# Kernel tuning notes

Measured on AMD Instinct MI355X. Metric: run time of the kernel, lower is better.

Reference implementation:

```python
import jax, jax.numpy as jnp
import numpy as np

N = 100000
E = 1600000
IN_DIM = 128
HID = 64
HEADS = 1
NEG_SLOPE = 0.2


def setup_inputs() -> dict:
    key = jax.random.key(0)
    ks = jax.random.split(key, 12)
    x = jax.random.normal(ks[0], (N, IN_DIM), dtype=jnp.float32)
    edge_index = jax.random.randint(ks[1], (2, E), 0, N, dtype=jnp.int64)
    s1 = 1.0 / np.sqrt(IN_DIM)
    s2 = 1.0 / np.sqrt(HEADS * HID)
    return {
        "x": x,
        "edge_index": edge_index,
        # layer 1: in_dim -> heads*hid
        "W1": jax.random.normal(ks[2], (IN_DIM, HEADS * HID), dtype=jnp.float32) * s1,
        "a_src1": jax.random.normal(ks[3], (HEADS, HID), dtype=jnp.float32) * s1,
        "a_dst1": jax.random.normal(ks[4], (HEADS, HID), dtype=jnp.float32) * s1,
        "b1": jnp.zeros((HEADS * HID,), dtype=jnp.float32),
        # layer 2: heads*hid -> hid (1 head)
        "W2": jax.random.normal(ks[5], (HEADS * HID, HID), dtype=jnp.float32) * s2,
        "a_src2": jax.random.normal(ks[6], (1, HID), dtype=jnp.float32) * s2,
        "a_dst2": jax.random.normal(ks[7], (1, HID), dtype=jnp.float32) * s2,
        "b2": jnp.zeros((HID,), dtype=jnp.float32),
        # output head
        "W_out": jax.random.normal(ks[8], (HID, 1), dtype=jnp.float32) * (1.0 / np.sqrt(HID)),
        "b_out": jnp.zeros((1,), dtype=jnp.float32),
    }


def _gat_conv(x, src, dst, W, a_src, a_dst, bias, heads, hid):
    n = x.shape[0]
    h = (x @ W).reshape(n, heads, hid)                      # [N, H, D]
    alpha_s = jnp.einsum("nhd,hd->nh", h, a_src)            # [N, H]
    alpha_d = jnp.einsum("nhd,hd->nh", h, a_dst)
    e = alpha_s[src] + alpha_d[dst]                          # [E, H]
    e = jax.nn.leaky_relu(e, NEG_SLOPE)
    # segment softmax over edges sharing the same destination node
    m = jax.ops.segment_max(e, dst, num_segments=n)          # [N, H]
    ex = jnp.exp(e - m[dst])
    denom = jax.ops.segment_sum(ex, dst, num_segments=n)     # [N, H]
    alpha = ex / denom[dst]                                  # [E, H]
    out = jax.ops.segment_sum(h[src] * alpha[:, :, None], dst, num_segments=n)
    return out.reshape(n, heads * hid) + bias


def reference(x, edge_index, W1, a_src1, a_dst1, b1, W2, a_src2, a_dst2, b2, W_out, b_out):
    n = x.shape[0]
    # PyG GATConv default add_self_loops=True
    loops = jnp.arange(n, dtype=edge_index.dtype)
    src = jnp.concatenate([edge_index[0], loops])
    dst = jnp.concatenate([edge_index[1], loops])
    h = jax.nn.elu(_gat_conv(x, src, dst, W1, a_src1, a_dst1, b1, HEADS, HID))
    h = jax.nn.elu(_gat_conv(h, src, dst, W2, a_src2, a_dst2, b2, 1, HID))
    return (h @ W_out + b_out).squeeze(-1)                   # [N]
```

## Files before the change

kernel.cpp:

```cpp
#include <hip/hip_runtime.h>
#include <hip/hip_fp16.h>
#include <math.h>

#define NEG_SLOPE 0.2f
#define BKT_SHIFT 8
#define BKT_NODES (1 << BKT_SHIFT)
#define BKT_CAP 512
#define BKT_FCAP 6144
#define BKT_SHARD (BKT_FCAP / 4)
#define P1_CHUNK 4096

typedef _Float16 f16x8 __attribute__((ext_vector_type(8)));
typedef float    f32x4 __attribute__((ext_vector_type(4)));
union FU  { uint4 u; f16x8 f; };
union H2U { __half2 h; unsigned u; };

__device__ __forceinline__ float lrelu(float x){ return fmaxf(x, NEG_SLOPE * x); }
__device__ __forceinline__ float elu_fast(float x){
  float t = __expf(fminf(x, 0.f)) - 1.f;
  return x > 0.f ? x : t;
}


__global__ __launch_bounds__(256) void k_p1(const int* __restrict__ src, const int* __restrict__ dst,
                                            int E, int B, int* __restrict__ bktCur,
                                            unsigned* __restrict__ pairs,
                                            const float* __restrict__ W1, const float* __restrict__ W2,
                                            uint4* __restrict__ W1f, uint4* __restrict__ W2f){
  __shared__ int h[BKT_CAP], base[BKT_CAP], cur[BKT_CAP];
  int tid = threadIdx.x;
  if (blockIdx.x == 0){
    for (int idx = tid; idx < 16 * 64; idx += 256){
      int lane = idx & 63, fs = idx >> 6;
      int t = fs >> 2, s = fs & 3;
      int m = lane & 15, quad = lane >> 4;
      f16x8 v;
      #pragma unroll
      for (int j = 0; j < 8; ++j)
        v[j] = (_Float16)W1[(s * 32 + quad * 8 + j) * 64 + t * 16 + m];
      FU fu; fu.f = v;
      W1f[fs * 64 + lane] = fu.u;
    }
    for (int idx = tid; idx < 8 * 64; idx += 256){
      int lane = idx & 63, fs = idx >> 6;
      int t = fs >> 1, s = fs & 1;
      int m = lane & 15, quad = lane >> 4;
      f16x8 v;
      #pragma unroll
      for (int j = 0; j < 8; ++j)
        v[j] = (_Float16)W2[(s * 32 + quad * 8 + j) * 64 + t * 16 + m];
      FU fu; fu.f = v;
      W2f[fs * 64 + lane] = fu.u;
    }
  }
  for (int i = tid; i < BKT_CAP; i += 256){ h[i] = 0; cur[i] = 0; }
  __syncthreads();
  int beg = blockIdx.x * P1_CHUNK;
  int end = min(beg + P1_CHUNK, E);
  int shard = blockIdx.x & 3;
  int m4 = (end - beg) >> 2;
  const int4* d4 = (const int4*)(dst + beg);
  const int4* s4 = (const int4*)(src + beg);
  for (int i = tid; i < m4; i += 256){
    int4 d = d4[i];
    atomicAdd(&h[d.x >> BKT_SHIFT], 1); atomicAdd(&h[d.y >> BKT_SHIFT], 1);
    atomicAdd(&h[d.z >> BKT_SHIFT], 1); atomicAdd(&h[d.w >> BKT_SHIFT], 1);
  }
  for (int i = beg + (m4 << 2) + tid; i < end; i += 256)
    atomicAdd(&h[dst[i] >> BKT_SHIFT], 1);
  __syncthreads();
  for (int i = tid; i < B; i += 256)
    if (h[i]) base[i] = i * BKT_FCAP + shard * BKT_SHARD + atomicAdd(&bktCur[i * 4 + shard], h[i]);
  __syncthreads();
  for (int i = tid; i < m4; i += 256){
    int4 d = d4[i]; int4 s = s4[i];
    int b0 = d.x >> BKT_SHIFT, b1 = d.y >> BKT_SHIFT, b2 = d.z >> BKT_SHIFT, b3 = d.w >> BKT_SHIFT;
    int p0 = base[b0] + atomicAdd(&cur[b0], 1);
    pairs[p0] = ((unsigned)(d.x & (BKT_NODES-1)) << 17) | (unsigned)s.x;
    int p1 = base[b1] + atomicAdd(&cur[b1], 1);
    pairs[p1] = ((unsigned)(d.y & (BKT_NODES-1)) << 17) | (unsigned)s.y;
    int p2 = base[b2] + atomicAdd(&cur[b2], 1);
    pairs[p2] = ((unsigned)(d.z & (BKT_NODES-1)) << 17) | (unsigned)s.z;
    int p3 = base[b3] + atomicAdd(&cur[b3], 1);
    pairs[p3] = ((unsigned)(d.w & (BKT_NODES-1)) << 17) | (unsigned)s.w;
  }
  for (int i = beg + (m4 << 2) + tid; i < end; i += 256){
    int d = dst[i], s = src[i];
    int b = d >> BKT_SHIFT;
    int p = base[b] + atomicAdd(&cur[b], 1);
    pairs[p] = ((unsigned)(d & (BKT_NODES-1)) << 17) | (unsigned)s;
  }
}

__device__ __forceinline__ void p2_body(const unsigned* __restrict__ pairs,
                                        const int* __restrict__ bktCur,
                                        int N, int2* __restrict__ offs2, int* __restrict__ col, int b){
  __shared__ int sc[BKT_NODES], cu[BKT_NODES];
  int tid = threadIdx.x;
  int nbase = b << BKT_SHIFT;
  int bs = b * BKT_FCAP;
  sc[tid] = 0;
  __syncthreads();
  #pragma unroll
  for (int s = 0; s < 4; ++s){
    int ss_ = bs + s * BKT_SHARD;
    int se_ = ss_ + bktCur[b * 4 + s];
    for (int i = ss_ + tid; i < se_; i += 256)
      atomicAdd(&sc[pairs[i] >> 17], 1);
  }
  __syncthreads();
  int v = sc[tid];
  for (int o = 1; o < 256; o <<= 1){
    int x = (tid >= o) ? sc[tid - o] : 0;
    __syncthreads();
    sc[tid] += x;
    __syncthreads();
  }
  int ex = sc[tid] - v;
  cu[tid] = bs + ex;
  if (nbase + tid < N) offs2[nbase + tid] = make_int2(bs + ex, bs + ex + v);
  __syncthreads();
  #pragma unroll
  for (int s = 0; s < 4; ++s){
    int ss_ = bs + s * BKT_SHARD;
    int se_ = ss_ + bktCur[b * 4 + s];
    for (int i = ss_ + tid; i < se_; i += 256){
      unsigned pr = pairs[i];
      int p = atomicAdd(&cu[pr >> 17], 1);
      col[p] = (int)(pr & 0x1FFFFu);
    }
  }
}

__device__ __forceinline__ void mg1_body(
    const float* __restrict__ X, const uint4* __restrict__ Wf,
    const float* __restrict__ a_src, const float* __restrict__ a_dst,
    uint2* __restrict__ H, float* __restrict__ as_, float* __restrict__ ad_, int n, int bb)
{
  int lane = threadIdx.x & 63, wv = threadIdx.x >> 6;
  int quad = lane >> 4, nn = lane & 15;
  int rowb = bb * 64 + wv * 16;
  int row = rowb + nn;
  bool ok = row < n;
  int rowc = ok ? row : n - 1;

  f16x8 af[4][4];
  #pragma unroll
  for (int t = 0; t < 4; ++t)
    #pragma unroll
    for (int s = 0; s < 4; ++s){
      FU fu; fu.u = Wf[(t * 4 + s) * 64 + lane];
      af[t][s] = fu.f;
    }

  const float4* Xr = (const float4*)(X + (size_t)rowc * 128);
  float4 xb[4][2];
  #pragma unroll
  for (int s = 0; s < 4; ++s){
    xb[s][0] = Xr[s * 8 + quad * 2];
    xb[s][1] = Xr[s * 8 + quad * 2 + 1];
  }

  f32x4 acc[4] = {};
  #pragma unroll
  for (int s = 0; s < 4; ++s){
    f16x8 bf;
    bf[0] = (_Float16)xb[s][0].x; bf[1] = (_Float16)xb[s][0].y;
    bf[2] = (_Float16)xb[s][0].z; bf[3] = (_Float16)xb[s][0].w;
    bf[4] = (_Float16)xb[s][1].x; bf[5] = (_Float16)xb[s][1].y;
    bf[6] = (_Float16)xb[s][1].z; bf[7] = (_Float16)xb[s][1].w;
    #pragma unroll
    for (int t = 0; t < 4; ++t)
      acc[t] = __builtin_amdgcn_mfma_f32_16x16x32_f16(af[t][s], bf, acc[t], 0, 0, 0);
  }

  if (ok){
    #pragma unroll
    for (int t = 0; t < 4; ++t){
      H2U p0, p1;
      p0.h = __floats2half2_rn(acc[t][0], acc[t][1]);
      p1.h = __floats2half2_rn(acc[t][2], acc[t][3]);
      H[(size_t)row * 16 + t * 4 + quad] = make_uint2(p0.u, p1.u);
    }
  }
  float sl = 0.f, dl = 0.f;
  #pragma unroll
  for (int t = 0; t < 4; ++t){
    float4 a4 = ((const float4*)a_src)[t * 4 + quad];
    float4 d4 = ((const float4*)a_dst)[t * 4 + quad];
    sl += acc[t][0] * a4.x + acc[t][1] * a4.y + acc[t][2] * a4.z + acc[t][3] * a4.w;
    dl += acc[t][0] * d4.x + acc[t][1] * d4.y + acc[t][2] * d4.z + acc[t][3] * d4.w;
  }
  sl += __shfl_xor(sl, 16, 64); sl += __shfl_xor(sl, 32, 64);
  dl += __shfl_xor(dl, 16, 64); dl += __shfl_xor(dl, 32, 64);
  if (lane < 16 && ok){ as_[row] = sl; ad_[row] = dl; }
}

__global__ __launch_bounds__(256) void k_fused(
    const unsigned* __restrict__ pairs, const int* __restrict__ bktCur,
    int N, int2* __restrict__ offs2, int* __restrict__ col, int p2B,
    const float* __restrict__ X, const uint4* __restrict__ Wf,
    const float* __restrict__ a_src, const float* __restrict__ a_dst,
    uint2* __restrict__ H, float* __restrict__ as_, float* __restrict__ ad_)
{
  if ((int)blockIdx.x < p2B)
    p2_body(pairs, bktCur, N, offs2, col, blockIdx.x);
  else
    mg1_body(X, Wf, a_src, a_dst, H, as_, ad_, N, blockIdx.x - p2B);
}

#define FMA8(e, hv) { const __half2* hp = (const __half2*)&(hv);               \
  a[0]=fmaf(e, __half2float(hp[0].x), a[0]); a[1]=fmaf(e, __half2float(hp[0].y), a[1]); \
  a[2]=fmaf(e, __half2float(hp[1].x), a[2]); a[3]=fmaf(e, __half2float(hp[1].y), a[3]); \
  a[4]=fmaf(e, __half2float(hp[2].x), a[4]); a[5]=fmaf(e, __half2float(hp[2].y), a[5]); \
  a[6]=fmaf(e, __half2float(hp[3].x), a[6]); a[7]=fmaf(e, __half2float(hp[3].y), a[7]); }

__device__ __forceinline__ void agg_core(
    const int2* __restrict__ offs2, const int* __restrict__ col,
    const uint4* __restrict__ H4, const float* __restrict__ as_, const float* __restrict__ ad_,
    int node, int c8, float& denom, float a[8])
{
  int2 be2 = offs2[node];
  int beg = be2.x, d = be2.y - be2.x;
  int maxd = d;
  maxd = max(maxd, __shfl_xor(maxd, 8, 64));
  maxd = max(maxd, __shfl_xor(maxd, 16, 64));
  maxd = max(maxd, __shfl_xor(maxd, 32, 64));
  float adv = ad_[node];
  float exs = __expf(lrelu(as_[node] + adv));
  uint4 hself = H4[(size_t)node * 8 + c8];
  denom = exs;
  { const __half2* hp = (const __half2*)&hself;
    #pragma unroll
    for (int i = 0; i < 4; ++i){
      a[2*i]   = exs * __half2float(hp[i].x);
      a[2*i+1] = exs * __half2float(hp[i].y);
    } }
  for (int j = 0; j < maxd; j += 4){
    int ss[4]; float asv[4]; uint4 hv[4];
    #pragma unroll
    for (int u = 0; u < 4; ++u) ss[u] = (j + u < d) ? col[beg + j + u] : 0;
    #pragma unroll
    for (int u = 0; u < 4; ++u) asv[u] = as_[ss[u]];
    #pragma unroll
    for (int u = 0; u < 4; ++u) hv[u] = H4[(size_t)ss[u] * 8 + c8];
    #pragma unroll
    for (int u = 0; u < 4; ++u){
      float e = (j + u < d) ? __expf(lrelu(asv[u] + adv)) : 0.f;
      denom += e;
      FMA8(e, hv[u])
    }
  }
}

__global__ __launch_bounds__(256) void k_agg1f(
    const int2* __restrict__ offs2, const int* __restrict__ col,
    const uint4* __restrict__ H4, const float* __restrict__ as_, const float* __restrict__ ad_,
    const float* __restrict__ bias, const uint4* __restrict__ W2f,
    const float* __restrict__ a_src2, const float* __restrict__ a_dst2,
    uint2* __restrict__ H2out, float* __restrict__ as2_, float* __restrict__ ad2_, int n)
{
  __shared__ unsigned uhl[32][36];
  int lane = threadIdx.x & 63, w = threadIdx.x >> 6;
  int m = lane >> 3, c8 = lane & 7;
  int node0 = blockIdx.x * 32 + w * 8 + m;
  bool ok = node0 < n;
  int node = ok ? node0 : n - 1;
  float denom; float a[8];
  agg_core(offs2, col, H4, as_, ad_, node, c8, denom, a);
  float inv = 1.f / denom;
  float4 b0 = *(const float4*)&bias[8 * c8];
  float4 b1 = *(const float4*)&bias[8 * c8 + 4];
  float bb[8] = {b0.x, b0.y, b0.z, b0.w, b1.x, b1.y, b1.z, b1.w};
  int ln = w * 8 + m;
  #pragma unroll
  for (int i = 0; i < 4; ++i){
    float v0 = elu_fast(fmaf(a[2*i],   inv, bb[2*i]));
    float v1 = elu_fast(fmaf(a[2*i+1], inv, bb[2*i+1]));
    __half2 h = __floats2half2_rn(v0, v1);
    uhl[ln][c8 * 4 + i] = *(unsigned*)&h;
  }
  __syncthreads();

  if (w < 2){
    int quad = lane >> 4, nn = lane & 15;
    int lrow = w * 16 + nn;
    int row = blockIdx.x * 32 + lrow;
    bool ok2 = row < n;

    f16x8 af[4][2];
    #pragma unroll
    for (int t = 0; t < 4; ++t)
      #pragma unroll
      for (int s = 0; s < 2; ++s){
        FU fu; fu.u = W2f[(t * 2 + s) * 64 + lane];
        af[t][s] = fu.f;
      }

    f16x8 bf[2];
    #pragma unroll
    for (int s = 0; s < 2; ++s){
      FU fu; fu.u = ((const uint4*)&uhl[lrow][0])[s * 4 + quad];
      bf[s] = fu.f;
    }

    f32x4 acc[4] = {};
    #pragma unroll
    for (int s = 0; s < 2; ++s)
      #pragma unroll
      for (int t = 0; t < 4; ++t)
        acc[t] = __builtin_amdgcn_mfma_f32_16x16x32_f16(af[t][s], bf[s], acc[t], 0, 0, 0);

    if (ok2){
      #pragma unroll
      for (int t = 0; t < 4; ++t){
        H2U p0, p1;
        p0.h = __floats2half2_rn(acc[t][0], acc[t][1]);
        p1.h = __floats2half2_rn(acc[t][2], acc[t][3]);
        H2out[(size_t)row * 16 + t * 4 + quad] = make_uint2(p0.u, p1.u);
      }
    }
    float sl = 0.f, dl = 0.f;
    #pragma unroll
    for (int t = 0; t < 4; ++t){
      float4 a4 = ((const float4*)a_src2)[t * 4 + quad];
      float4 d4 = ((const float4*)a_dst2)[t * 4 + quad];
      sl += acc[t][0] * a4.x + acc[t][1] * a4.y + acc[t][2] * a4.z + acc[t][3] * a4.w;
      dl += acc[t][0] * d4.x + acc[t][1] * d4.y + acc[t][2] * d4.z + acc[t][3] * d4.w;
    }
    sl += __shfl_xor(sl, 16, 64); sl += __shfl_xor(sl, 32, 64);
    dl += __shfl_xor(dl, 16, 64); dl += __shfl_xor(dl, 32, 64);
    if (lane < 16 && ok2){ as2_[row] = sl; ad2_[row] = dl; }
  }
}

__global__ __launch_bounds__(256) void k_agg2(
    const int2* __restrict__ offs2, const int* __restrict__ col,
    const uint4* __restrict__ H4, const float* __restrict__ as_, const float* __restrict__ ad_,
    const float* __restrict__ bias, const float* __restrict__ Wout, const float* __restrict__ bout,
    float* __restrict__ out, int n)
{
  int lane = threadIdx.x & 63, w = threadIdx.x >> 6;
  int m = lane >> 3, c8 = lane & 7;
  int node0 = blockIdx.x * 32 + w * 8 + m;
  bool ok = node0 < n;
  int node = ok ? node0 : n - 1;
  float denom; float a[8];
  agg_core(offs2, col, H4, as_, ad_, node, c8, denom, a);
  float inv = 1.f / denom;
  float4 b0 = *(const float4*)&bias[8 * c8];
  float4 b1 = *(const float4*)&bias[8 * c8 + 4];
  float4 w0 = *(const float4*)&Wout[8 * c8];
  float4 w1 = *(const float4*)&Wout[8 * c8 + 4];
  float bb[8] = {b0.x, b0.y, b0.z, b0.w, b1.x, b1.y, b1.z, b1.w};
  float ww[8] = {w0.x, w0.y, w0.z, w0.w, w1.x, w1.y, w1.z, w1.w};
  float p = 0.f;
  #pragma unroll
  for (int i = 0; i < 8; ++i)
    p += elu_fast(fmaf(a[i], inv, bb[i])) * ww[i];
  p += __shfl_xor(p, 1, 64); p += __shfl_xor(p, 2, 64); p += __shfl_xor(p, 4, 64);
  if (c8 == 0 && ok) out[node] = p + bout[0];
}

extern "C" void kernel_launch(void* const* d_in, const int* in_sizes, int n_in,
                              void* d_out, int out_size, void* d_ws, size_t ws_size,
                              hipStream_t stream)
{
  const float* x    = (const float*)d_in[0];
  const int*   ei   = (const int*)d_in[1];
  const float* W1   = (const float*)d_in[2];
  const float* as1w = (const float*)d_in[3];
  const float* ad1w = (const float*)d_in[4];
  const float* b1   = (const float*)d_in[5];
  const float* W2   = (const float*)d_in[6];
  const float* as2w = (const float*)d_in[7];
  const float* ad2w = (const float*)d_in[8];
  const float* b2   = (const float*)d_in[9];
  const float* Wout = (const float*)d_in[10];
  const float* bout = (const float*)d_in[11];
  float* out = (float*)d_out;

  const int N = in_sizes[0] / 128;
  const int E = in_sizes[1] / 2;
  const int* srcA = ei;
  const int* dstA = ei + E;
  const int B = (N + BKT_NODES - 1) >> BKT_SHIFT;

  char* p = (char*)d_ws;
  auto alloc = [&](size_t bytes){ char* r = p; p += (bytes + 255) & ~255ull; return r; };
  int*   bktCur = (int*)alloc(BKT_CAP * 4 * 4);
  int2*  offs2  = (int2*)alloc((size_t)N * 8);
  int*   col    = (int*)alloc((size_t)B * BKT_FCAP * 4);
  float* vas1 = (float*)alloc((size_t)N * 4);
  float* vad1 = (float*)alloc((size_t)N * 4);
  float* vas2 = (float*)alloc((size_t)N * 4);
  float* vad2 = (float*)alloc((size_t)N * 4);
  uint4* w1f  = (uint4*)alloc(16 * 64 * 16);
  uint4* w2f  = (uint4*)alloc(8 * 64 * 16);
  uint2* h1   = (uint2*)alloc((size_t)N * 64 * 2);
  uint2* h2   = (uint2*)alloc((size_t)N * 64 * 2);
  unsigned* pairs = (unsigned*)h2;

  hipMemsetAsync(bktCur, 0, BKT_CAP * 4 * 4, stream);

  int nchunk = (E + P1_CHUNK - 1) / P1_CHUNK;
  k_p1<<<nchunk, 256, 0, stream>>>(srcA, dstA, E, B, bktCur, pairs, W1, W2, w1f, w2f);

  int gblocks = (N + 63) / 64;
  int ablocks = (N + 31) / 32;
  k_fused<<<B + gblocks, 256, 0, stream>>>(pairs, bktCur, N, offs2, col, B,
                                           x, w1f, as1w, ad1w, h1, vas1, vad1);
  k_agg1f <<<ablocks, 256, 0, stream>>>(offs2, col, (const uint4*)h1, vas1, vad1, b1,
                                        w2f, as2w, ad2w, h2, vas2, vad2, N);
  k_agg2  <<<ablocks, 256, 0, stream>>>(offs2, col, (const uint4*)h2, vas2, vad2, b2, Wout, bout, out, N);
}
```

Before: 234.8 us.

## Replace global bucket atomics with per-chunk local sort and offset table

The edge bucketing pass now sorts each chunk's edges by bucket in shared memory, using a block-wide prefix scan over a 512-entry histogram. It writes them contiguously per chunk together with a per-chunk bucket offset table, which removes the global atomic counters and the memset. The CSR build pass then gathers each bucket's segments from all chunks through that offset table into shared memory before counting and scattering. This replaces the scattered global writes with coalesced ones, at the cost of a per-bucket gather of roughly 391 short segments read serially by each thread, plus larger shared-memory staging.

```diff
diff --git a/kernel.cpp b/kernel.cpp
--- a/kernel.cpp
+++ b/kernel.cpp
@@ -5,9 +5,7 @@
 #define NEG_SLOPE 0.2f
 #define BKT_SHIFT 8
 #define BKT_NODES (1 << BKT_SHIFT)
-#define BKT_CAP 512
 #define BKT_FCAP 6144
-#define BKT_SHARD (BKT_FCAP / 4)
 #define P1_CHUNK 4096
 
 typedef _Float16 f16x8 __attribute__((ext_vector_type(8)));
@@ -21,16 +19,16 @@
   return x > 0.f ? x : t;
 }
 
-
-__global__ __launch_bounds__(256) void k_p1(const int* __restrict__ src, const int* __restrict__ dst,
-                                            int E, int B, int* __restrict__ bktCur,
-                                            unsigned* __restrict__ pairs,
+__global__ __launch_bounds__(512) void k_p1(const int* __restrict__ src, const int* __restrict__ dst,
+                                            int E, int B,
+                                            unsigned* __restrict__ pairs, int* __restrict__ offsT,
                                             const float* __restrict__ W1, const float* __restrict__ W2,
                                             uint4* __restrict__ W1f, uint4* __restrict__ W2f){
-  __shared__ int h[BKT_CAP], base[BKT_CAP], cur[BKT_CAP];
+  __shared__ int h[512], cur[512];
+  __shared__ unsigned stage[P1_CHUNK];
   int tid = threadIdx.x;
   if (blockIdx.x == 0){
-    for (int idx = tid; idx < 16 * 64; idx += 256){
+    for (int idx = tid; idx < 16 * 64; idx += 512){
       int lane = idx & 63, fs = idx >> 6;
       int t = fs >> 2, s = fs & 3;
       int m = lane & 15, quad = lane >> 4;
@@ -41,7 +39,7 @@
       FU fu; fu.f = v;
       W1f[fs * 64 + lane] = fu.u;
     }
-    for (int idx = tid; idx < 8 * 64; idx += 256){
+    for (int idx = tid; idx < 8 * 64; idx += 512){
       int lane = idx & 63, fs = idx >> 6;
       int t = fs >> 1, s = fs & 1;
       int m = lane & 15, quad = lane >> 4;
@@ -53,61 +51,84 @@
       W2f[fs * 64 + lane] = fu.u;
     }
   }
-  for (int i = tid; i < BKT_CAP; i += 256){ h[i] = 0; cur[i] = 0; }
+  h[tid] = 0;
   __syncthreads();
   int beg = blockIdx.x * P1_CHUNK;
   int end = min(beg + P1_CHUNK, E);
-  int shard = blockIdx.x & 3;
-  int m4 = (end - beg) >> 2;
+  int cnt = end - beg;
+  int m4 = cnt >> 2;
   const int4* d4 = (const int4*)(dst + beg);
   const int4* s4 = (const int4*)(src + beg);
-  for (int i = tid; i < m4; i += 256){
+  for (int i = tid; i < m4; i += 512){
     int4 d = d4[i];
     atomicAdd(&h[d.x >> BKT_SHIFT], 1); atomicAdd(&h[d.y >> BKT_SHIFT], 1);
     atomicAdd(&h[d.z >> BKT_SHIFT], 1); atomicAdd(&h[d.w >> BKT_SHIFT], 1);
   }
-  for (int i = beg + (m4 << 2) + tid; i < end; i += 256)
-    atomicAdd(&h[dst[i] >> BKT_SHIFT], 1);
-  __syncthreads();
-  for (int i = tid; i < B; i += 256)
-    if (h[i]) base[i] = i * BKT_FCAP + shard * BKT_SHARD + atomicAdd(&bktCur[i * 4 + shard], h[i]);
-  __syncthreads();
-  for (int i = tid; i < m4; i += 256){
+  for (int i = (m4 << 2) + tid; i < cnt; i += 512)
+    atomicAdd(&h[dst[beg + i] >> BKT_SHIFT], 1);
+  __syncthreads();
+  int v = h[tid];
+  for (int o = 1; o < 512; o <<= 1){
+    int x = (tid >= o) ? h[tid - o] : 0;
+    __syncthreads();
+    h[tid] += x;
+    __syncthreads();
+  }
+  int e = h[tid] - v;
+  cur[tid] = e;
+  int* orow = offsT + (size_t)blockIdx.x * (B + 1);
+  if (tid <= B) orow[tid] = e;
+  __syncthreads();
+  for (int i = tid; i < m4; i += 512){
     int4 d = d4[i]; int4 s = s4[i];
-    int b0 = d.x >> BKT_SHIFT, b1 = d.y >> BKT_SHIFT, b2 = d.z >> BKT_SHIFT, b3 = d.w >> BKT_SHIFT;
-    int p0 = base[b0] + atomicAdd(&cur[b0], 1);
-    pairs[p0] = ((unsigned)(d.x & (BKT_NODES-1)) << 17) | (unsigned)s.x;
-    int p1 = base[b1] + atomicAdd(&cur[b1], 1);
-    pairs[p1] = ((unsigned)(d.y & (BKT_NODES-1)) << 17) | (unsigned)s.y;
-    int p2 = base[b2] + atomicAdd(&cur[b2], 1);
-    pairs[p2] = ((unsigned)(d.z & (BKT_NODES-1)) << 17) | (unsigned)s.z;
-    int p3 = base[b3] + atomicAdd(&cur[b3], 1);
-    pairs[p3] = ((unsigned)(d.w & (BKT_NODES-1)) << 17) | (unsigned)s.w;
-  }
-  for (int i = beg + (m4 << 2) + tid; i < end; i += 256){
-    int d = dst[i], s = src[i];
-    int b = d >> BKT_SHIFT;
-    int p = base[b] + atomicAdd(&cur[b], 1);
-    pairs[p] = ((unsigned)(d & (BKT_NODES-1)) << 17) | (unsigned)s;
-  }
+    int p0 = atomicAdd(&cur[d.x >> BKT_SHIFT], 1);
+    stage[p0] = ((unsigned)(d.x & (BKT_NODES-1)) << 17) | (unsigned)s.x;
+    int p1 = atomicAdd(&cur[d.y >> BKT_SHIFT], 1);
+    stage[p1] = ((unsigned)(d.y & (BKT_NODES-1)) << 17) | (unsigned)s.y;
+    int p2 = atomicAdd(&cur[d.z >> BKT_SHIFT], 1);
+    stage[p2] = ((unsigned)(d.z & (BKT_NODES-1)) << 17) | (unsigned)s.z;
+    int p3 = atomicAdd(&cur[d.w >> BKT_SHIFT], 1);
+    stage[p3] = ((unsigned)(d.w & (BKT_NODES-1)) << 17) | (unsigned)s.w;
+  }
+  for (int i = (m4 << 2) + tid; i < cnt; i += 512){
+    int d = dst[beg + i], s = src[beg + i];
+    int p = atomicAdd(&cur[d >> BKT_SHIFT], 1);
+    stage[p] = ((unsigned)(d & (BKT_NODES-1)) << 17) | (unsigned)s;
+  }
+  __syncthreads();
+  unsigned* prow = pairs + (size_t)blockIdx.x * P1_CHUNK;
+  for (int i = tid; i < cnt; i += 512) prow[i] = stage[i];
 }
 
 __device__ __forceinline__ void p2_body(const unsigned* __restrict__ pairs,
-                                        const int* __restrict__ bktCur,
-                                        int N, int2* __restrict__ offs2, int* __restrict__ col, int b){
-  __shared__ int sc[BKT_NODES], cu[BKT_NODES];
+                                        const int* __restrict__ offsT,
+                                        int NCH, int B, int N,
+                                        int2* __restrict__ offs2, int* __restrict__ col, int b){
+  __shared__ int sc[BKT_NODES], cu[BKT_NODES], rbase[512];
+  __shared__ unsigned estage[BKT_FCAP];
   int tid = threadIdx.x;
   int nbase = b << BKT_SHIFT;
   int bs = b * BKT_FCAP;
+  int i0 = tid, i1 = tid + 256;
+  int st0 = 0, ln0 = 0, st1 = 0, ln1 = 0;
+  if (i0 < NCH){ int o = offsT[(size_t)i0 * (B + 1) + b]; st0 = o; ln0 = offsT[(size_t)i0 * (B + 1) + b + 1] - o; }
+  if (i1 < NCH){ int o = offsT[(size_t)i1 * (B + 1) + b]; st1 = o; ln1 = offsT[(size_t)i1 * (B + 1) + b + 1] - o; }
+  rbase[tid] = ln0; rbase[tid + 256] = ln1;
   sc[tid] = 0;
   __syncthreads();
-  #pragma unroll
-  for (int s = 0; s < 4; ++s){
-    int ss_ = bs + s * BKT_SHARD;
-    int se_ = ss_ + bktCur[b * 4 + s];
-    for (int i = ss_ + tid; i < se_; i += 256)
-      atomicAdd(&sc[pairs[i] >> 17], 1);
-  }
+  for (int o = 1; o < 512; o <<= 1){
+    int x0 = (tid >= o) ? rbase[tid - o] : 0;
+    int x1 = rbase[tid + 256 - o];
+    __syncthreads();
+    rbase[tid] += x0; rbase[tid + 256] += x1;
+    __syncthreads();
+  }
+  int tot = rbase[511];
+  int r0 = rbase[tid] - ln0, r1 = rbase[tid + 256] - ln1;
+  for (int j = 0; j < ln0; ++j) estage[r0 + j] = pairs[(size_t)i0 * P1_CHUNK + st0 + j];
+  for (int j = 0; j < ln1; ++j) estage[r1 + j] = pairs[(size_t)i1 * P1_CHUNK + st1 + j];
+  __syncthreads();
+  for (int i = tid; i < tot; i += 256) atomicAdd(&sc[estage[i] >> 17], 1);
   __syncthreads();
   int v = sc[tid];
   for (int o = 1; o < 256; o <<= 1){
@@ -120,15 +141,10 @@
   cu[tid] = bs + ex;
   if (nbase + tid < N) offs2[nbase + tid] = make_int2(bs + ex, bs + ex + v);
   __syncthreads();
-  #pragma unroll
-  for (int s = 0; s < 4; ++s){
-    int ss_ = bs + s * BKT_SHARD;
-    int se_ = ss_ + bktCur[b * 4 + s];
-    for (int i = ss_ + tid; i < se_; i += 256){
-      unsigned pr = pairs[i];
-      int p = atomicAdd(&cu[pr >> 17], 1);
-      col[p] = (int)(pr & 0x1FFFFu);
-    }
+  for (int i = tid; i < tot; i += 256){
+    unsigned pr = estage[i];
+    int p = atomicAdd(&cu[pr >> 17], 1);
+    col[p] = (int)(pr & 0x1FFFFu);
   }
 }
 
@@ -197,16 +213,16 @@
 }
 
 __global__ __launch_bounds__(256) void k_fused(
-    const unsigned* __restrict__ pairs, const int* __restrict__ bktCur,
-    int N, int2* __restrict__ offs2, int* __restrict__ col, int p2B,
+    const unsigned* __restrict__ pairs, const int* __restrict__ offsT,
+    int NCH, int B, int N, int2* __restrict__ offs2, int* __restrict__ col,
     const float* __restrict__ X, const uint4* __restrict__ Wf,
     const float* __restrict__ a_src, const float* __restrict__ a_dst,
     uint2* __restrict__ H, float* __restrict__ as_, float* __restrict__ ad_)
 {
-  if ((int)blockIdx.x < p2B)
-    p2_body(pairs, bktCur, N, offs2, col, blockIdx.x);
+  if ((int)blockIdx.x < B)
+    p2_body(pairs, offsT, NCH, B, N, offs2, col, blockIdx.x);
   else
-    mg1_body(X, Wf, a_src, a_dst, H, as_, ad_, N, blockIdx.x - p2B);
+    mg1_body(X, Wf, a_src, a_dst, H, as_, ad_, N, blockIdx.x - B);
 }
 
 #define FMA8(e, hv) { const __half2* hp = (const __half2*)&(hv);               \
@@ -384,13 +400,14 @@
   const int E = in_sizes[1] / 2;
   const int* srcA = ei;
   const int* dstA = ei + E;
-  const int B = (N + BKT_NODES - 1) >> BKT_SHIFT;
+  const int B   = (N + BKT_NODES - 1) >> BKT_SHIFT;
+  const int NCH = (E + P1_CHUNK - 1) / P1_CHUNK;
 
   char* p = (char*)d_ws;
   auto alloc = [&](size_t bytes){ char* r = p; p += (bytes + 255) & ~255ull; return r; };
-  int*   bktCur = (int*)alloc(BKT_CAP * 4 * 4);
   int2*  offs2  = (int2*)alloc((size_t)N * 8);
   int*   col    = (int*)alloc((size_t)B * BKT_FCAP * 4);
+  int*   offsT  = (int*)alloc((size_t)NCH * (B + 1) * 4);
   float* vas1 = (float*)alloc((size_t)N * 4);
   float* vad1 = (float*)alloc((size_t)N * 4);
   float* vas2 = (float*)alloc((size_t)N * 4);
@@ -401,14 +418,11 @@
   uint2* h2   = (uint2*)alloc((size_t)N * 64 * 2);
   unsigned* pairs = (unsigned*)h2;
 
-  hipMemsetAsync(bktCur, 0, BKT_CAP * 4 * 4, stream);
-
-  int nchunk = (E + P1_CHUNK - 1) / P1_CHUNK;
-  k_p1<<<nchunk, 256, 0, stream>>>(srcA, dstA, E, B, bktCur, pairs, W1, W2, w1f, w2f);
+  k_p1<<<NCH, 512, 0, stream>>>(srcA, dstA, E, B, pairs, offsT, W1, W2, w1f, w2f);
 
   int gblocks = (N + 63) / 64;
   int ablocks = (N + 31) / 32;
-  k_fused<<<B + gblocks, 256, 0, stream>>>(pairs, bktCur, N, offs2, col, B,
+  k_fused<<<B + gblocks, 256, 0, stream>>>(pairs, offsT, NCH, B, N, offs2, col,
                                            x, w1f, as1w, ad1w, h1, vas1, vad1);
   k_agg1f <<<ablocks, 256, 0, stream>>>(offs2, col, (const uint4*)h1, vas1, vad1, b1,
                                         w2f, as2w, ad2w, h2, vas2, vad2, N);
```

After: 222.6 us. 5.2% less time.
